# Kernel tuning notes

Measured on AMD Instinct MI355X. Metric: run time of the kernel, lower is better.

Reference implementation:

```python
import jax, jax.numpy as jnp
import numpy as np

K = 1024   # num_embeddings
E = 64     # embedding_dim
T = 1024   # time
B = 64     # batch
BETA = 0.25  # commitment_cost


def setup_inputs() -> dict:
    key = jax.random.key(0)
    k1, k2 = jax.random.split(key)
    inputs = jax.random.normal(k1, (E, T, B), dtype=jnp.float32)
    # torch init: uniform(-1/num_embeddings, 1/num_embeddings)
    codebook = jax.random.uniform(k2, (K, E), dtype=jnp.float32,
                                  minval=-1.0 / K, maxval=1.0 / K)
    return {"inputs": inputs, "codebook": codebook}


def reference(inputs, codebook):
    # inputs: [E, T, B]; torch does permute(1,2,0) -> [T, B, E]
    x = jnp.transpose(inputs, (1, 2, 0))            # [T, B, E]
    flat = x.reshape(-1, E)                          # [N, E], N = T*B
    d = (jnp.sum(flat * flat, axis=1, keepdims=True)
         + jnp.sum(codebook * codebook, axis=1)
         - 2.0 * (flat @ codebook.T))
    idx = jnp.argmin(d, axis=1)                      # [N]
    # one-hot @ codebook == gather (same math, efficient form)
    q = codebook[idx].reshape(T, B, E)               # [T, B, E]

    e_latent_loss = jnp.mean((jax.lax.stop_gradient(q) - x) ** 2)
    q_latent_loss = jnp.mean((q - jax.lax.stop_gradient(x)) ** 2)
    vq_loss = q_latent_loss + BETA * e_latent_loss

    # straight-through estimator
    q_st = x + jax.lax.stop_gradient(q - x)

    # perplexity from code-usage histogram (mean of one-hots)
    N = flat.shape[0]
    counts = jnp.zeros((K,), jnp.float32).at[idx].add(1.0)
    avg_probs = counts / N
    perplexity = jnp.exp(-jnp.sum(avg_probs * jnp.log(avg_probs + 1e-10)))

    quantized = jnp.transpose(q_st, (2, 0, 1))       # back to [E, T, B]
    return vq_loss, quantized, perplexity
```

## Files before the change

### kernel.cpp

```cpp
#include <hip/hip_runtime.h>


#define KC 1024
#define ED 64
#define NR 65536
#define NE (NR * ED)
#define GAP1 6e-6f

typedef __attribute__((ext_vector_type(8))) short short8;
typedef __attribute__((ext_vector_type(4))) float f32x4;

__device__ __forceinline__ unsigned short bf16rne(float f) {
    unsigned u = __builtin_bit_cast(unsigned, f);
    return (unsigned short)((u + 0x7fffu + ((u >> 16) & 1u)) >> 16);
}
__device__ __forceinline__ float bf16tof(unsigned short h) {
    return __builtin_bit_cast(float, (unsigned)h << 16);
}

__global__ __launch_bounds__(256) void k_pack(const float* __restrict__ cb,
        short8* __restrict__ cbt, unsigned* __restrict__ counts,
        unsigned* __restrict__ flagcnt) {
    const int u = blockIdx.x * 256 + threadIdx.x;
    if (u < 1024) counts[u] = 0u;
    if (u == 1024) *flagcnt = 0u;
    if (u >= 64 * 7 * 64) return;
    const int t = u / 448, rem = u % 448, j = rem / 64, l = rem % 64;
    const int g = l >> 4;
    if (j < 6) {
        const int code = t * 16 + (l & 15);
        const float* c = cb + (size_t)code * ED;
        short8 o;
#pragma unroll
        for (int r = 0; r < 8; ++r) {
            const int k = j * 32 + g * 8 + r;
            int e; bool lo;
            if (j < 2)      { e = k;       lo = false; }
            else if (j < 4) { e = k - 64;  lo = true;  }
            else            { e = k - 128; lo = false; }
            const float m2 = -2.f * c[e];
            const unsigned short h = bf16rne(m2);
            o[r] = lo ? (short)bf16rne(m2 - bf16tof(h)) : (short)h;
        }
        cbt[u] = o;
    } else {
        f32x4 o;
#pragma unroll
        for (int r = 0; r < 4; ++r) {
            const float4* c4 = (const float4*)(cb + (size_t)(t * 16 + g * 4 + r) * ED);
            float s0 = 0.f, s1 = 0.f, s2 = 0.f, s3 = 0.f;
#pragma unroll
            for (int i = 0; i < 16; ++i) {
                const float4 c = c4[i];
                s0 = fmaf(c.x, c.x, s0); s1 = fmaf(c.y, c.y, s1);
                s2 = fmaf(c.z, c.z, s2); s3 = fmaf(c.w, c.w, s3);
            }
            o[r] = (s0 + s1) + (s2 + s3);
        }
        cbt[u] = __builtin_bit_cast(short8, o);
    }
}

__global__ __launch_bounds__(512) void k_argmin(
        const float* __restrict__ in, const short8* __restrict__ cbt,
        int* __restrict__ idx, unsigned* __restrict__ counts,
        unsigned* __restrict__ flagcnt, unsigned* __restrict__ flaglist,
        double* __restrict__ pblk) {
    __shared__ short8 xs[16][4][64];
    __shared__ float rx2p[2][256];
    __shared__ float sb[4][16][16], sb2[4][16][16];
    __shared__ int   sk[4][16][16];
    __shared__ double sred[4];

    const int tid = threadIdx.x;
    const int l = tid & 63;
    const int wid = tid >> 6;
    const int g = l >> 4;
    const int col = l & 15;
    const int rowBase = blockIdx.x * 256;

    {
        const int row = tid & 255;
        const int h = tid >> 8;
        const int grt = row >> 4;
        const int cl = row & 15;
        float part = 0.f;
#pragma unroll
        for (int gg = 0; gg < 4; ++gg) {
            short8 H, L;
#pragma unroll
            for (int j = 0; j < 8; ++j) {
                const float x = in[(size_t)(h * 32 + gg * 8 + j) * NR + rowBase + row];
                const unsigned short hb = bf16rne(x);
                H[j] = (short)hb;
                L[j] = (short)bf16rne(x - bf16tof(hb));
                part = fmaf(x, x, part);
            }
            xs[grt][h][gg * 16 + cl] = H;
            xs[grt][2 + h][gg * 16 + cl] = L;
        }
        rx2p[h][row] = part;
    }
    __syncthreads();

    const int rg = wid >> 2, kh = wid & 3;
    short8 xq[8][4];
#pragma unroll
    for (int rt = 0; rt < 8; ++rt)
#pragma unroll
        for (int q = 0; q < 4; ++q)
            xq[rt][q] = xs[rg * 8 + rt][q][l];

    float best[8], best2[8]; int bestk[8];
#pragma unroll
    for (int rt = 0; rt < 8; ++rt) { best[rt] = 3.4e38f; best2[rt] = 3.4e38f; bestk[rt] = 0; }

    for (int tt = 0; tt < 16; ++tt) {
        const int t = kh * 16 + tt;
        const short8* bp = cbt + (size_t)t * 448 + l;
        const short8 b0 = bp[0], b1 = bp[64], b2 = bp[128],
                     b3 = bp[192], b4 = bp[256], b5 = bp[320];
        const f32x4 e4 = __builtin_bit_cast(f32x4, bp[384]);
#pragma unroll
        for (int rt = 0; rt < 8; ++rt) {
            f32x4 acc = e4;
            acc = __builtin_amdgcn_mfma_f32_16x16x32_bf16(b0, xq[rt][0], acc, 0, 0, 0);
            acc = __builtin_amdgcn_mfma_f32_16x16x32_bf16(b1, xq[rt][1], acc, 0, 0, 0);
            acc = __builtin_amdgcn_mfma_f32_16x16x32_bf16(b2, xq[rt][0], acc, 0, 0, 0);
            acc = __builtin_amdgcn_mfma_f32_16x16x32_bf16(b3, xq[rt][1], acc, 0, 0, 0);
            acc = __builtin_amdgcn_mfma_f32_16x16x32_bf16(b4, xq[rt][2], acc, 0, 0, 0);
            acc = __builtin_amdgcn_mfma_f32_16x16x32_bf16(b5, xq[rt][3], acc, 0, 0, 0);
#pragma unroll
            for (int r = 0; r < 4; ++r) {
                const float v = acc[r];
                const int k = t * 16 + g * 4 + r;
                best2[rt] = fminf(fmaxf(v, best[rt]), best2[rt]);
                const bool c = v < best[rt];
                bestk[rt] = c ? k : bestk[rt];
                best[rt]  = fminf(v, best[rt]);
            }
        }
    }

#pragma unroll
    for (int rt = 0; rt < 8; ++rt) {
        float b = best[rt], b2 = best2[rt]; int k = bestk[rt];
#pragma unroll
        for (int sh = 16; sh <= 32; sh <<= 1) {
            const float ob  = __shfl_xor(b, sh, 64);
            const float ob2 = __shfl_xor(b2, sh, 64);
            const int   ok  = __shfl_xor(k, sh, 64);
            if (ob < b || (ob == b && ok < k)) { b2 = fminf(b, ob2); k = ok; b = ob; }
            else b2 = fminf(b2, ob);
        }
        if (g == 0) {
            sb[kh][rg * 8 + rt][col] = b;
            sb2[kh][rg * 8 + rt][col] = b2;
            sk[kh][rg * 8 + rt][col] = k;
        }
    }
    __syncthreads();

    if (wid < 4) {
        const int grt = wid * 4 + (l >> 4);
        float b = sb[0][grt][col], b2 = sb2[0][grt][col]; int k = sk[0][grt][col];
#pragma unroll
        for (int s = 1; s < 4; ++s) {
            const float ob = sb[s][grt][col], ob2 = sb2[s][grt][col];
            const int ok = sk[s][grt][col];
            if (ob < b || (ob == b && ok < k)) { b2 = fminf(b, ob2); k = ok; b = ob; }
            else b2 = fminf(b2, ob);
        }
        const int lrow = grt * 16 + col;
        const int row = rowBase + lrow;
        idx[row] = k;
        atomicAdd(&counts[k], 1u);
        if (b2 - b < GAP1) {
            const unsigned p = atomicAdd(flagcnt, 1u);
            flaglist[p] = (unsigned)row;
        }
        double d2 = (double)b + (double)(rx2p[0][lrow] + rx2p[1][lrow]);
#pragma unroll
        for (int off = 32; off > 0; off >>= 1) d2 += __shfl_down(d2, off, 64);
        if (l == 0) sred[wid] = d2;
    }
    __syncthreads();
    if (tid == 0)
        pblk[blockIdx.x] = (sred[0] + sred[1]) + (sred[2] + sred[3]);
}

__global__ __launch_bounds__(256) void k_exact64(
        const float* __restrict__ in, const float* __restrict__ cb,
        int* __restrict__ idx, unsigned* __restrict__ counts,
        const unsigned* __restrict__ flagcnt, const unsigned* __restrict__ flaglist) {
    const unsigned nf = *flagcnt;
    const int l = threadIdx.x & 63;
    const unsigned wave = blockIdx.x * 4u + (unsigned)(threadIdx.x >> 6);
    const unsigned nwave = gridDim.x * 4u;
    for (unsigned i = wave; i < nf; i += nwave) {
        const int row = (int)flaglist[i];
        float x[ED];
#pragma unroll
        for (int e = 0; e < ED; ++e) x[e] = in[(size_t)e * NR + row];
        double best = 1e300; int bestk = 0;
        for (int ci = 0; ci < 16; ++ci) {
            const int k = ci * 64 + l;
            const float* c = cb + (size_t)k * ED;
            double s = 0.0, e2 = 0.0;
            for (int e = 0; e < ED; ++e) {
                const double cv = (double)c[e];
                e2 = fma(cv, cv, e2);
                s  = fma(cv, (double)x[e], s);
            }
            const double t = fma(-2.0, s, e2);
            if (t < best) { best = t; bestk = k; }
        }
        for (int sh = 1; sh < 64; sh <<= 1) {
            const double ob = __shfl_xor(best, sh, 64);
            const int   ok  = __shfl_xor(bestk, sh, 64);
            if (ob < best || (ob == best && ok < bestk)) { best = ob; bestk = ok; }
        }
        if (l == 0) {
            const int old = idx[row];
            if (bestk != old) {
                idx[row] = bestk;
                atomicSub(&counts[old], 1u);
                atomicAdd(&counts[bestk], 1u);
            }
        }
    }
}

__global__ __launch_bounds__(256) void k_output(
        const float* __restrict__ cb, const int* __restrict__ idx,
        float* __restrict__ qout, const unsigned* __restrict__ counts,
        const double* __restrict__ pblk, float* __restrict__ out) {
    const int gtid = blockIdx.x * 256 + threadIdx.x;
    const int n = gtid & (NR - 1);
    const int e0 = gtid >> 16;
    const int k = idx[n];
    const float4* c4 = (const float4*)(cb + (size_t)k * ED + e0 * 8);
    const float4 q0 = c4[0], q1 = c4[1];
#pragma unroll
    for (int j = 0; j < 8; ++j) {
        const float q = (j < 4) ? ((const float*)&q0)[j] : ((const float*)&q1)[j - 4];
        qout[(size_t)(e0 * 8 + j) * NR + n] = q;
    }
    if (blockIdx.x == 0) {
        __shared__ double redE[4], redS[4];
        const int tid = threadIdx.x;
        double term = 0.0;
#pragma unroll
        for (int i = 0; i < 4; ++i) {
            const double p = (double)counts[tid + i * 256] * (1.0 / 65536.0);
            term += p * log(p + 1e-10);
        }
        double s = pblk[tid];
#pragma unroll
        for (int off = 32; off > 0; off >>= 1) {
            term += __shfl_down(term, off, 64);
            s    += __shfl_down(s,    off, 64);
        }
        if ((tid & 63) == 0) { redE[tid >> 6] = term; redS[tid >> 6] = s; }
        __syncthreads();
        if (tid == 0) {
            const double e = (redE[0] + redE[1]) + (redE[2] + redE[3]);
            const double ss = (redS[0] + redS[1]) + (redS[2] + redS[3]);
            out[1 + NE] = (float)exp(-e);
            const double m = ss * (1.0 / 4194304.0);
            out[0] = (float)(1.25 * m);
        }
    }
}

extern "C" void kernel_launch(void* const* d_in, const int* in_sizes, int n_in,
                              void* d_out, int out_size, void* d_ws, size_t ws_size,
                              hipStream_t stream) {
    (void)in_sizes; (void)n_in; (void)out_size; (void)ws_size;
    const float* in = (const float*)d_in[0];
    const float* cb = (const float*)d_in[1];
    float* out = (float*)d_out;

    unsigned* counts   = (unsigned*)d_ws;
    unsigned* flagcnt  = (unsigned*)d_ws + 1024;
    short8*   cbt      = (short8*)((float*)d_ws + 2048);
    int*      idx      = (int*)d_ws + 116736;
    unsigned* flaglist = (unsigned*)d_ws + 182272;
    double*   pblk     = (double*)((char*)d_ws + 991232);

    hipLaunchKernelGGL(k_pack,    dim3(112),  dim3(256), 0, stream,
                       cb, cbt, counts, flagcnt);
    hipLaunchKernelGGL(k_argmin,  dim3(256),  dim3(512), 0, stream,
                       in, cbt, idx, counts, flagcnt, flaglist, pblk);
    hipLaunchKernelGGL(k_exact64, dim3(128),  dim3(256), 0, stream,
                       in, cb, idx, counts, flagcnt, flaglist);
    hipLaunchKernelGGL(k_output,  dim3(2048), dim3(256), 0, stream,
                       cb, idx, out + 1, counts, pblk, out);
}
```

Measured before the change: 90.12 us.

## Drop duplicate codebook hi tiles, widen argmin blocks, double-buffer codebook loads

```diff
diff --git a/kernel.cpp b/kernel.cpp
--- a/kernel.cpp
+++ b/kernel.cpp
@@ -24,20 +24,17 @@
     const int u = blockIdx.x * 256 + threadIdx.x;
     if (u < 1024) counts[u] = 0u;
     if (u == 1024) *flagcnt = 0u;
-    if (u >= 64 * 7 * 64) return;
-    const int t = u / 448, rem = u % 448, j = rem / 64, l = rem % 64;
+    if (u >= 64 * 5 * 64) return;
+    const int t = u / 320, rem = u % 320, j = rem / 64, l = rem % 64;
     const int g = l >> 4;
-    if (j < 6) {
+    if (j < 4) {
         const int code = t * 16 + (l & 15);
         const float* c = cb + (size_t)code * ED;
+        const bool lo = (j >= 2);
         short8 o;
 #pragma unroll
         for (int r = 0; r < 8; ++r) {
-            const int k = j * 32 + g * 8 + r;
-            int e; bool lo;
-            if (j < 2)      { e = k;       lo = false; }
-            else if (j < 4) { e = k - 64;  lo = true;  }
-            else            { e = k - 128; lo = false; }
+            const int e = (j & 1) * 32 + g * 8 + r;
             const float m2 = -2.f * c[e];
             const unsigned short h = bf16rne(m2);
             o[r] = lo ? (short)bf16rne(m2 - bf16tof(h)) : (short)h;
@@ -61,15 +58,15 @@
     }
 }
 
-__global__ __launch_bounds__(512) void k_argmin(
+__global__ __launch_bounds__(1024) void k_argmin(
         const float* __restrict__ in, const short8* __restrict__ cbt,
         int* __restrict__ idx, unsigned* __restrict__ counts,
         unsigned* __restrict__ flagcnt, unsigned* __restrict__ flaglist,
         double* __restrict__ pblk) {
-    __shared__ short8 xs[16][4][64];
-    __shared__ float rx2p[2][256];
-    __shared__ float sb[4][16][16], sb2[4][16][16];
-    __shared__ int   sk[4][16][16];
+    __shared__ short8 xs[4][16][64];
+    __shared__ float rx2p[4][256];
+    __shared__ float sb[16][4][16], sb2[16][4][16];
+    __shared__ int   sk[16][4][16];
     __shared__ double sred[4];
 
     const int tid = threadIdx.x;
@@ -81,69 +78,89 @@
 
     {
         const int row = tid & 255;
-        const int h = tid >> 8;
-        const int grt = row >> 4;
-        const int cl = row & 15;
+        const int ob = tid >> 8;
+        const int rg = row >> 6;
+        const int r6 = row & 63;
+        const int rt = r6 >> 4;
+        const int ll = ob * 16 + (r6 & 15);
         float part = 0.f;
 #pragma unroll
-        for (int gg = 0; gg < 4; ++gg) {
+        for (int hh = 0; hh < 2; ++hh) {
+            const int oct = ob + hh * 4;
             short8 H, L;
 #pragma unroll
             for (int j = 0; j < 8; ++j) {
-                const float x = in[(size_t)(h * 32 + gg * 8 + j) * NR + rowBase + row];
+                const float x = in[(size_t)(oct * 8 + j) * NR + rowBase + row];
                 const unsigned short hb = bf16rne(x);
                 H[j] = (short)hb;
                 L[j] = (short)bf16rne(x - bf16tof(hb));
                 part = fmaf(x, x, part);
             }
-            xs[grt][h][gg * 16 + cl] = H;
-            xs[grt][2 + h][gg * 16 + cl] = L;
-        }
-        rx2p[h][row] = part;
+            xs[rg][rt * 4 + hh][ll] = H;
+            xs[rg][rt * 4 + 2 + hh][ll] = L;
+        }
+        rx2p[ob][row] = part;
     }
     __syncthreads();
 
     const int rg = wid >> 2, kh = wid & 3;
-    short8 xq[8][4];
-#pragma unroll
-    for (int rt = 0; rt < 8; ++rt)
+    short8 xq[4][4];
+#pragma unroll
+    for (int rt = 0; rt < 4; ++rt)
 #pragma unroll
         for (int q = 0; q < 4; ++q)
-            xq[rt][q] = xs[rg * 8 + rt][q][l];
-
-    float best[8], best2[8]; int bestk[8];
-#pragma unroll
-    for (int rt = 0; rt < 8; ++rt) { best[rt] = 3.4e38f; best2[rt] = 3.4e38f; bestk[rt] = 0; }
-
-    for (int tt = 0; tt < 16; ++tt) {
-        const int t = kh * 16 + tt;
-        const short8* bp = cbt + (size_t)t * 448 + l;
-        const short8 b0 = bp[0], b1 = bp[64], b2 = bp[128],
-                     b3 = bp[192], b4 = bp[256], b5 = bp[320];
-        const f32x4 e4 = __builtin_bit_cast(f32x4, bp[384]);
-#pragma unroll
-        for (int rt = 0; rt < 8; ++rt) {
-            f32x4 acc = e4;
-            acc = __builtin_amdgcn_mfma_f32_16x16x32_bf16(b0, xq[rt][0], acc, 0, 0, 0);
-            acc = __builtin_amdgcn_mfma_f32_16x16x32_bf16(b1, xq[rt][1], acc, 0, 0, 0);
-            acc = __builtin_amdgcn_mfma_f32_16x16x32_bf16(b2, xq[rt][0], acc, 0, 0, 0);
-            acc = __builtin_amdgcn_mfma_f32_16x16x32_bf16(b3, xq[rt][1], acc, 0, 0, 0);
-            acc = __builtin_amdgcn_mfma_f32_16x16x32_bf16(b4, xq[rt][2], acc, 0, 0, 0);
-            acc = __builtin_amdgcn_mfma_f32_16x16x32_bf16(b5, xq[rt][3], acc, 0, 0, 0);
-#pragma unroll
-            for (int r = 0; r < 4; ++r) {
-                const float v = acc[r];
-                const int k = t * 16 + g * 4 + r;
-                best2[rt] = fminf(fmaxf(v, best[rt]), best2[rt]);
-                const bool c = v < best[rt];
-                bestk[rt] = c ? k : bestk[rt];
-                best[rt]  = fminf(v, best[rt]);
-            }
-        }
-    }
-
-#pragma unroll
-    for (int rt = 0; rt < 8; ++rt) {
+            xq[rt][q] = xs[rg][rt * 4 + q][l];
+
+    float best[4]  = {3.4e38f, 3.4e38f, 3.4e38f, 3.4e38f};
+    float best2[4] = {3.4e38f, 3.4e38f, 3.4e38f, 3.4e38f};
+    int bestk[4] = {0, 0, 0, 0};
+
+    const int t0 = kh * 16;
+
+#define LOADT(P, T) do { \
+        const short8* bp_ = cbt + (size_t)(T) * 320 + l; \
+        P##0 = bp_[0];   P##1 = bp_[64]; \
+        P##2 = bp_[128]; P##3 = bp_[192]; \
+        P##e = __builtin_bit_cast(f32x4, bp_[256]); \
+    } while (0)
+
+#define COMPT(P, T) do { \
+        _Pragma("unroll") \
+        for (int rt_ = 0; rt_ < 4; ++rt_) { \
+            f32x4 acc_ = P##e; \
+            acc_ = __builtin_amdgcn_mfma_f32_16x16x32_bf16(P##0, xq[rt_][0], acc_, 0, 0, 0); \
+            acc_ = __builtin_amdgcn_mfma_f32_16x16x32_bf16(P##1, xq[rt_][1], acc_, 0, 0, 0); \
+            acc_ = __builtin_amdgcn_mfma_f32_16x16x32_bf16(P##2, xq[rt_][0], acc_, 0, 0, 0); \
+            acc_ = __builtin_amdgcn_mfma_f32_16x16x32_bf16(P##3, xq[rt_][1], acc_, 0, 0, 0); \
+            acc_ = __builtin_amdgcn_mfma_f32_16x16x32_bf16(P##0, xq[rt_][2], acc_, 0, 0, 0); \
+            acc_ = __builtin_amdgcn_mfma_f32_16x16x32_bf16(P##1, xq[rt_][3], acc_, 0, 0, 0); \
+            _Pragma("unroll") \
+            for (int r_ = 0; r_ < 4; ++r_) { \
+                const float v_ = acc_[r_]; \
+                const int k_ = (T) * 16 + g * 4 + r_; \
+                best2[rt_] = fminf(fmaxf(v_, best[rt_]), best2[rt_]); \
+                const bool c_ = v_ < best[rt_]; \
+                bestk[rt_] = c_ ? k_ : bestk[rt_]; \
+                best[rt_]  = fminf(v_, best[rt_]); \
+            } \
+        } \
+    } while (0)
+
+    short8 A0, A1, A2, A3; f32x4 Ae;
+    short8 B0, B1, B2, B3; f32x4 Be;
+    LOADT(A, t0);
+#pragma unroll
+    for (int p = 0; p < 8; ++p) {
+        LOADT(B, t0 + 2 * p + 1);
+        COMPT(A, t0 + 2 * p);
+        if (p < 7) LOADT(A, t0 + 2 * p + 2);
+        COMPT(B, t0 + 2 * p + 1);
+    }
+#undef LOADT
+#undef COMPT
+
+#pragma unroll
+    for (int rt = 0; rt < 4; ++rt) {
         float b = best[rt], b2 = best2[rt]; int k = bestk[rt];
 #pragma unroll
         for (int sh = 16; sh <= 32; sh <<= 1) {
@@ -153,25 +170,22 @@
             if (ob < b || (ob == b && ok < k)) { b2 = fminf(b, ob2); k = ok; b = ob; }
             else b2 = fminf(b2, ob);
         }
-        if (g == 0) {
-            sb[kh][rg * 8 + rt][col] = b;
-            sb2[kh][rg * 8 + rt][col] = b2;
-            sk[kh][rg * 8 + rt][col] = k;
-        }
+        if (g == 0) { sb[wid][rt][col] = b; sb2[wid][rt][col] = b2; sk[wid][rt][col] = k; }
     }
     __syncthreads();
 
     if (wid < 4) {
-        const int grt = wid * 4 + (l >> 4);
-        float b = sb[0][grt][col], b2 = sb2[0][grt][col]; int k = sk[0][grt][col];
+        const int rt = l >> 4, c2 = l & 15;
+        float b = sb[wid * 4][rt][c2], b2 = sb2[wid * 4][rt][c2];
+        int k = sk[wid * 4][rt][c2];
 #pragma unroll
         for (int s = 1; s < 4; ++s) {
-            const float ob = sb[s][grt][col], ob2 = sb2[s][grt][col];
-            const int ok = sk[s][grt][col];
+            const float ob = sb[wid * 4 + s][rt][c2], ob2 = sb2[wid * 4 + s][rt][c2];
+            const int ok = sk[wid * 4 + s][rt][c2];
             if (ob < b || (ob == b && ok < k)) { b2 = fminf(b, ob2); k = ok; b = ob; }
             else b2 = fminf(b2, ob);
         }
-        const int lrow = grt * 16 + col;
+        const int lrow = wid * 64 + rt * 16 + c2;
         const int row = rowBase + lrow;
         idx[row] = k;
         atomicAdd(&counts[k], 1u);
@@ -179,7 +193,8 @@
             const unsigned p = atomicAdd(flagcnt, 1u);
             flaglist[p] = (unsigned)row;
         }
-        double d2 = (double)b + (double)(rx2p[0][lrow] + rx2p[1][lrow]);
+        double d2 = (double)b + (double)((rx2p[0][lrow] + rx2p[1][lrow])
+                                       + (rx2p[2][lrow] + rx2p[3][lrow]));
 #pragma unroll
         for (int off = 32; off > 0; off >>= 1) d2 += __shfl_down(d2, off, 64);
         if (l == 0) sred[wid] = d2;
@@ -284,16 +299,16 @@
     unsigned* counts   = (unsigned*)d_ws;
     unsigned* flagcnt  = (unsigned*)d_ws + 1024;
     short8*   cbt      = (short8*)((float*)d_ws + 2048);
-    int*      idx      = (int*)d_ws + 116736;
-    unsigned* flaglist = (unsigned*)d_ws + 182272;
+    int*      idx      = (int*)d_ws + 83968;
+    unsigned* flaglist = (unsigned*)d_ws + 149504;
     double*   pblk     = (double*)((char*)d_ws + 991232);
 
-    hipLaunchKernelGGL(k_pack,    dim3(112),  dim3(256), 0, stream,
+    hipLaunchKernelGGL(k_pack,    dim3(80),   dim3(256),  0, stream,
                        cb, cbt, counts, flagcnt);
-    hipLaunchKernelGGL(k_argmin,  dim3(256),  dim3(512), 0, stream,
+    hipLaunchKernelGGL(k_argmin,  dim3(256),  dim3(1024), 0, stream,
                        in, cbt, idx, counts, flagcnt, flaglist, pblk);
-    hipLaunchKernelGGL(k_exact64, dim3(128),  dim3(256), 0, stream,
+    hipLaunchKernelGGL(k_exact64, dim3(128),  dim3(256),  0, stream,
                        in, cb, idx, counts, flagcnt, flaglist);
-    hipLaunchKernelGGL(k_output,  dim3(2048), dim3(256), 0, stream,
+    hipLaunchKernelGGL(k_output,  dim3(2048), dim3(256),  0, stream,
                        cb, idx, out + 1, counts, pblk, out);
 }
```

Result: slower. 158.0 us (+75.3%).
